# Kernel tuning notes

Measured on AMD Instinct MI355X. Metric: run time of the kernel, lower is better.

The kernel has to match this reference:

```python
import jax, jax.numpy as jnp
import numpy as np

D_MODEL = 1024
N_HEADS = 16
DEPTH = D_MODEL // N_HEADS  # 64
BATCH, SEQ = 4, 2048


def setup_inputs() -> dict:
    key = jax.random.key(0)
    ks = jax.random.split(key, 8)
    x = jax.random.normal(ks[0], (BATCH, SEQ, D_MODEL), dtype=jnp.float32)
    # Per-head Dense(depth) weights stacked over heads: [H, d_model, depth]
    s = 1.0 / np.sqrt(D_MODEL)
    Wq = jax.random.normal(ks[1], (N_HEADS, D_MODEL, DEPTH), dtype=jnp.float32) * s
    Wk = jax.random.normal(ks[2], (N_HEADS, D_MODEL, DEPTH), dtype=jnp.float32) * s
    Wv = jax.random.normal(ks[3], (N_HEADS, D_MODEL, DEPTH), dtype=jnp.float32) * s
    bq = jnp.zeros((N_HEADS, DEPTH), dtype=jnp.float32)
    bk = jnp.zeros((N_HEADS, DEPTH), dtype=jnp.float32)
    bv = jnp.zeros((N_HEADS, DEPTH), dtype=jnp.float32)
    Wo = jax.random.normal(ks[4], (D_MODEL, D_MODEL), dtype=jnp.float32) * s
    bo = jnp.zeros((D_MODEL,), dtype=jnp.float32)
    return {"x": x, "Wq": Wq, "bq": bq, "Wk": Wk, "bk": bk,
            "Wv": Wv, "bv": bv, "Wo": Wo, "bo": bo}


def reference(x, Wq, bq, Wk, bk, Wv, bv, Wo, bo):
    # Per-head projections, batched over heads: [b, h, s, depth]
    q = jnp.einsum('bsd,hde->bhse', x, Wq) + bq[None, :, None, :]
    k = jnp.einsum('bsd,hde->bhse', x, Wk) + bk[None, :, None, :]
    v = jnp.einsum('bsd,hde->bhse', x, Wv) + bv[None, :, None, :]
    scale = 1.0 / jnp.sqrt(jnp.float32(DEPTH))
    scores = jnp.einsum('bhqe,bhke->bhqk', q, k) * scale  # [b, h, s, s]
    attn = jax.nn.softmax(scores, axis=-1)
    z = jnp.einsum('bhqk,bhke->bhqe', attn, v)  # [b, h, s, depth]
    # Concat heads along last axis (head-major order matches tf.concat of per-head outputs)
    multi_head = z.transpose(0, 2, 1, 3).reshape(BATCH, SEQ, D_MODEL)
    return multi_head @ Wo + bo
```

## Files before the change

kernel.cpp:

```cpp
#include <hip/hip_runtime.h>

typedef unsigned short u16;
typedef __bf16 bf16x8 __attribute__((ext_vector_type(8)));
typedef float f32x4 __attribute__((ext_vector_type(4)));
typedef float f32x16 __attribute__((ext_vector_type(16)));
typedef unsigned int u32x4 __attribute__((ext_vector_type(4)));
typedef unsigned int u32x2 __attribute__((ext_vector_type(2)));

__device__ __forceinline__ u16 f2b(float f) {
  union { float f; unsigned u; } v; v.f = f;
  return (u16)((v.u + 0x7fffu + ((v.u >> 16) & 1u)) >> 16);
}

__device__ __forceinline__ unsigned pkbf(float a, float b) {
#if __has_builtin(__builtin_amdgcn_cvt_pk_bf16_f32)
  typedef __bf16 bf16x2v __attribute__((ext_vector_type(2)));
  bf16x2v r = __builtin_amdgcn_cvt_pk_bf16_f32(a, b);
  return __builtin_bit_cast(unsigned, r);
#else
  unsigned ua = __builtin_bit_cast(unsigned, a) + 0x8000u;
  unsigned ub = __builtin_bit_cast(unsigned, b) + 0x8000u;
  return __builtin_amdgcn_perm(ub, ua, 0x07060302u);
#endif
}

__device__ __forceinline__ float fexp2(float x) {
#if __has_builtin(__builtin_amdgcn_exp2f)
  return __builtin_amdgcn_exp2f(x);
#else
  return exp2f(x);
#endif
}

__device__ __forceinline__ bf16x8 ldfrag(const u16* p) {
  u32x4 r = *(const u32x4*)p;
  return __builtin_bit_cast(bf16x8, r);
}

__device__ __forceinline__ void plswap(unsigned& dst, unsigned& src) {
  asm("v_permlane32_swap_b32 %0, %1" : "+v"(dst), "+v"(src));
}

__device__ __forceinline__ float sum16(const f32x16& v) {
  float a = (v[0] + v[1]) + (v[2] + v[3]);
  float b = (v[4] + v[5]) + (v[6] + v[7]);
  float c = (v[8] + v[9]) + (v[10] + v[11]);
  float d = (v[12] + v[13]) + (v[14] + v[15]);
  return (a + b) + (c + d);
}

__device__ __forceinline__ void build_frags(const f32x16& sc, bf16x8& fLo, bf16x8& fHi) {
  unsigned a0 = pkbf(sc[0], sc[1]);
  unsigned a1 = pkbf(sc[2], sc[3]);
  unsigned b0 = pkbf(sc[4], sc[5]);
  unsigned b1 = pkbf(sc[6], sc[7]);
  plswap(a0, b0);
  plswap(a1, b1);
  u32x4 f; f[0] = a0; f[1] = a1; f[2] = b0; f[3] = b1;
  fLo = __builtin_bit_cast(bf16x8, f);
  unsigned c0 = pkbf(sc[8], sc[9]);
  unsigned c1 = pkbf(sc[10], sc[11]);
  unsigned d0 = pkbf(sc[12], sc[13]);
  unsigned d1 = pkbf(sc[14], sc[15]);
  plswap(c0, d0);
  plswap(c1, d1);
  u32x4 g; g[0] = c0; g[1] = c1; g[2] = d0; g[3] = d1;
  fHi = __builtin_bit_cast(bf16x8, g);
}

#define GLOAD_LDS16(gp, lp)                                                        \
  __builtin_amdgcn_global_load_lds((const __attribute__((address_space(1))) void*)(gp), \
                                   (__attribute__((address_space(3))) void*)(lp), 16, 0, 0)

#define MFMA32(a, b, c) __builtin_amdgcn_mfma_f32_32x32x16_bf16((a), (b), (c), 0, 0, 0)

#define QSC 0.18033688011f


__global__ __launch_bounds__(256) void k_pack(const float* __restrict__ x,
                                              const float* __restrict__ Wq,
                                              const float* __restrict__ Wk,
                                              const float* __restrict__ Wv,
                                              const float* __restrict__ Wo,
                                              u16* __restrict__ xb,
                                              u16* __restrict__ wqkv,
                                              u16* __restrict__ wo_t) {
  const int bid = blockIdx.x, tid = threadIdx.x;
  if (bid < 4096) {
    int i = (bid * 256 + tid) * 8;
    float4 v0 = *(const float4*)(x + i);
    float4 v1 = *(const float4*)(x + i + 4);
    u32x4 o;
    o[0] = pkbf(v0.x, v0.y);
    o[1] = pkbf(v0.z, v0.w);
    o[2] = pkbf(v1.x, v1.y);
    o[3] = pkbf(v1.z, v1.w);
    *(u32x4*)(xb + i) = o;
    return;
  }
  __shared__ u16 tile[64][65];
  if (bid < 4864) {
    int b2 = bid - 4096;
    int p = b2 >> 8, rem = b2 & 255, h = rem >> 4, dt = rem & 15;
    const float* W = (p == 0) ? Wq : (p == 1) ? Wk : Wv;
    for (int i = tid; i < 4096; i += 256) {
      int d = i >> 6, e = i & 63;
      tile[e][d] = f2b(W[h * 65536 + (dt * 64 + d) * 64 + e]);
    }
    __syncthreads();
    for (int i = tid; i < 4096; i += 256) {
      int e = i >> 6, d = i & 63;
      wqkv[(size_t)(p * 1024 + h * 64 + e) * 1024 + dt * 64 + d] = tile[e][d];
    }
  } else {
    int b2 = bid - 4864;
    int kt = b2 >> 4, nt = b2 & 15;
    for (int i = tid; i < 4096; i += 256) {
      int dk = i >> 6, de = i & 63;
      tile[de][dk] = f2b(Wo[(size_t)(kt * 64 + dk) * 1024 + nt * 64 + de]);
    }
    __syncthreads();
    for (int i = tid; i < 4096; i += 256) {
      int de = i >> 6, dk = i & 63;
      wo_t[(size_t)(nt * 64 + de) * 1024 + kt * 64 + dk] = tile[de][dk];
    }
  }
}


template <bool SWAP>
__device__ __forceinline__ void gemm_core32(const u16* __restrict__ A, const u16* __restrict__ Bt,
                                            int row0, int col0, u16* As, u16* Bs, f32x16 acc[2][2]) {
  const int tid = threadIdx.x, w = tid >> 6, lane = tid & 63;
  const int l31 = lane & 31, hi = lane >> 5;
  const int wm = (w >> 1) * 64, wn = (w & 1) * 64;
  for (int k0 = 0; k0 < 1024; k0 += 32) {
#pragma unroll
    for (int i = 0; i < 2; i++) {
      int bse = (w * 2 + i) * 512;
      int flat = bse + lane * 8;
      int r = flat >> 5, c = flat & 31;
      GLOAD_LDS16(A + (size_t)(row0 + r) * 1024 + k0 + c, As + bse);
      GLOAD_LDS16(Bt + (size_t)(col0 + r) * 1024 + k0 + c, Bs + bse);
    }
    __syncthreads();
    bf16x8 af[2][2], bfr[2][2];
#pragma unroll
    for (int t = 0; t < 2; t++)
#pragma unroll
      for (int s = 0; s < 2; s++) {
        af[t][s] = ldfrag(As + (wm + t * 32 + l31) * 32 + s * 16 + hi * 8);
        bfr[t][s] = ldfrag(Bs + (wn + t * 32 + l31) * 32 + s * 16 + hi * 8);
      }
#pragma unroll
    for (int mt = 0; mt < 2; mt++)
#pragma unroll
      for (int nt = 0; nt < 2; nt++)
#pragma unroll
        for (int s = 0; s < 2; s++)
          acc[mt][nt] = SWAP ? MFMA32(bfr[nt][s], af[mt][s], acc[mt][nt])
                             : MFMA32(af[mt][s], bfr[nt][s], acc[mt][nt]);
    __syncthreads();
  }
}


__global__ __launch_bounds__(256) void k_gemm_qkv(const u16* __restrict__ xb, const u16* __restrict__ wt,
                                                  const float* __restrict__ bq, const float* __restrict__ bk,
                                                  const float* __restrict__ bv,
                                                  u16* __restrict__ qo, u16* __restrict__ ko,
                                                  u16* __restrict__ vto) {
  __shared__ u16 As[4096], Bs[4096];
  f32x16 acc[2][2];
#pragma unroll
  for (int a = 0; a < 2; a++)
#pragma unroll
    for (int b = 0; b < 2; b++)
#pragma unroll
      for (int r = 0; r < 16; r++) acc[a][b][r] = 0.f;

  const int row0 = blockIdx.x * 128, col0 = blockIdx.y * 128;
  const int p = blockIdx.y >> 3;
  const int colr = (blockIdx.y & 7) * 128;
  const int tid = threadIdx.x, w = tid >> 6, lane = tid & 63;
  const int l31 = lane & 31, hi = lane >> 5;
  const int wm = (w >> 1) * 64, wn = (w & 1) * 64;

  if (p == 2) {
    gemm_core32<true>(xb, wt, row0, col0, As, Bs, acc);
#pragma unroll
    for (int mt = 0; mt < 2; mt++) {
      int rb = row0 + wm + mt * 32;
      int b_ = rb >> 11;
      int s_ = (rb & 2047) + l31;
#pragma unroll
      for (int nt = 0; nt < 2; nt++) {
        int ebase = colr + wn + nt * 32;
#pragma unroll
        for (int g = 0; g < 4; g++) {
          float4 bvv = *(const float4*)(bv + ebase + g * 8 + hi * 4);
#pragma unroll
          for (int j = 0; j < 4; j++) {
            int rem = ebase + g * 8 + hi * 4 + j;
            int h = rem >> 6, e = rem & 63;
            float val = acc[mt][nt][g * 4 + j] + (&bvv.x)[j];
            vto[(((size_t)(b_ * 16 + h)) * 64 + e) * 2048 + s_] = f2b(val);
          }
        }
      }
    }
  } else {
    gemm_core32<false>(xb, wt, row0, col0, As, Bs, acc);
    u16* dst = (p == 0) ? qo : ko;
    const float* bias = (p == 0) ? bq : bk;
    const float qsc = (p == 0) ? QSC : 1.0f;
#pragma unroll
    for (int nt = 0; nt < 2; nt++) {
      int rem = colr + wn + nt * 32 + l31;
      int h = rem >> 6, e = rem & 63;
      float bval = bias[rem];
#pragma unroll
      for (int mt = 0; mt < 2; mt++) {
        int rb = row0 + wm + mt * 32;
        int b_ = rb >> 11, sb = rb & 2047;
        size_t obase = ((size_t)(b_ * 16 + h) * 2048) * 64 + e;
#pragma unroll
        for (int reg = 0; reg < 16; reg++) {
          int s_ = sb + (reg & 3) + 8 * (reg >> 2) + 4 * hi;
          float val = (acc[mt][nt][reg] + bval) * qsc;
          dst[obase + (size_t)s_ * 64] = f2b(val);
        }
      }
    }
  }
}


__global__ __launch_bounds__(256) void k_gemm_out(const u16* __restrict__ zb, const u16* __restrict__ wt,
                                                  const float* __restrict__ bo, float* __restrict__ out) {
  __shared__ u16 As[4096], Bs[4096];
  f32x16 acc[2][2];
#pragma unroll
  for (int a = 0; a < 2; a++)
#pragma unroll
    for (int b = 0; b < 2; b++)
#pragma unroll
      for (int r = 0; r < 16; r++) acc[a][b][r] = 0.f;

  const int row0 = blockIdx.x * 128, col0 = blockIdx.y * 128;
  gemm_core32<false>(zb, wt, row0, col0, As, Bs, acc);

  const int tid = threadIdx.x, w = tid >> 6, lane = tid & 63;
  const int l31 = lane & 31, hi = lane >> 5;
  const int wm = (w >> 1) * 64, wn = (w & 1) * 64;
#pragma unroll
  for (int nt = 0; nt < 2; nt++) {
    int c = col0 + wn + nt * 32 + l31;
    float bval = bo[c];
#pragma unroll
    for (int mt = 0; mt < 2; mt++) {
      int rb = row0 + wm + mt * 32;
#pragma unroll
      for (int reg = 0; reg < 16; reg++) {
        int r = rb + (reg & 3) + 8 * (reg >> 2) + 4 * hi;
        out[(size_t)r * 1024 + c] = acc[mt][nt][reg] + bval;
      }
    }
  }
}


__global__ __launch_bounds__(256, 2) void k_attn(const u16* __restrict__ q, const u16* __restrict__ k,
                                                 const u16* __restrict__ vt, u16* __restrict__ z) {
  __shared__ u16 Ks[2][64 * 72], Vs[2][64 * 72];
  const int tid = threadIdx.x, w = tid >> 6, lane = tid & 63;
  const int l31 = lane & 31, hi = lane >> 5;
  const int bh = blockIdx.y, s0 = blockIdx.x * 256;
  const size_t base = (size_t)bh * 2048 * 64;
  const int qrow0 = s0 + w * 64;

  bf16x8 qf[2][4];
#pragma unroll
  for (int u = 0; u < 2; u++) {
    const u16* qp = q + base + (size_t)(qrow0 + u * 32 + l31) * 64 + hi * 8;
#pragma unroll
    for (int ks = 0; ks < 4; ks++) qf[u][ks] = ldfrag(qp + ks * 16);
  }

  f32x16 accT[2][2];
  float ls[2] = {0.f, 0.f};
#pragma unroll
  for (int u = 0; u < 2; u++)
#pragma unroll
    for (int r = 0; r < 16; r++) { accT[u][0][r] = 0.f; accT[u][1][r] = 0.f; }

  const int srow = tid >> 3;
  const int scol = (tid & 7) * 8;
  const u16* kg = k + base;
  const u16* vg = vt + base;

  u32x4 kr0 = *(const u32x4*)(kg + (size_t)srow * 64 + scol);
  u32x4 kr1 = *(const u32x4*)(kg + (size_t)(srow + 32) * 64 + scol);
  u32x4 vr0 = *(const u32x4*)(vg + (size_t)srow * 2048 + scol);
  u32x4 vr1 = *(const u32x4*)(vg + (size_t)(srow + 32) * 2048 + scol);
  *(u32x4*)&Ks[0][srow * 72 + scol] = kr0;
  *(u32x4*)&Ks[0][(srow + 32) * 72 + scol] = kr1;
  *(u32x4*)&Vs[0][srow * 72 + scol] = vr0;
  *(u32x4*)&Vs[0][(srow + 32) * 72 + scol] = vr1;
  kr0 = *(const u32x4*)(kg + (size_t)(64 + srow) * 64 + scol);
  kr1 = *(const u32x4*)(kg + (size_t)(64 + srow + 32) * 64 + scol);
  vr0 = *(const u32x4*)(vg + (size_t)srow * 2048 + 64 + scol);
  vr1 = *(const u32x4*)(vg + (size_t)(srow + 32) * 2048 + 64 + scol);
  __syncthreads();

  for (int kc = 0; kc < 2048; kc += 64) {
    const int buf = (kc >> 6) & 1;
    const u16* Kb = &Ks[buf][0];
    const u16* Vb = &Vs[buf][0];

    bf16x8 pf[2][4];
#pragma unroll
    for (int t = 0; t < 2; t++) {
      f32x16 scA, scB;
#pragma unroll
      for (int r = 0; r < 16; r++) { scA[r] = 0.f; scB[r] = 0.f; }
      __builtin_amdgcn_s_setprio(1);
#pragma unroll
      for (int ks = 0; ks < 4; ks++) {
        bf16x8 kf = ldfrag(Kb + (t * 32 + l31) * 72 + ks * 16 + hi * 8);
        scA = MFMA32(kf, qf[0][ks], scA);
        scB = MFMA32(kf, qf[1][ks], scB);
      }
      __builtin_amdgcn_s_setprio(0);
#pragma unroll
      for (int r = 0; r < 16; r++) scA[r] = fexp2(scA[r]);
#pragma unroll
      for (int r = 0; r < 16; r++) scB[r] = fexp2(scB[r]);
      ls[0] += sum16(scA);
      ls[1] += sum16(scB);
      build_frags(scA, pf[0][2 * t], pf[0][2 * t + 1]);
      build_frags(scB, pf[1][2 * t], pf[1][2 * t + 1]);
    }

    if (kc + 64 < 2048) {
      *(u32x4*)&Ks[buf ^ 1][srow * 72 + scol] = kr0;
      *(u32x4*)&Ks[buf ^ 1][(srow + 32) * 72 + scol] = kr1;
      *(u32x4*)&Vs[buf ^ 1][srow * 72 + scol] = vr0;
      *(u32x4*)&Vs[buf ^ 1][(srow + 32) * 72 + scol] = vr1;
      if (kc + 128 < 2048) {
        int kn = kc + 128;
        kr0 = *(const u32x4*)(kg + (size_t)(kn + srow) * 64 + scol);
        kr1 = *(const u32x4*)(kg + (size_t)(kn + srow + 32) * 64 + scol);
        vr0 = *(const u32x4*)(vg + (size_t)srow * 2048 + kn + scol);
        vr1 = *(const u32x4*)(vg + (size_t)(srow + 32) * 2048 + kn + scol);
      }
    }

    __builtin_amdgcn_s_setprio(1);
#pragma unroll
    for (int ks = 0; ks < 4; ks++) {
      bf16x8 vf0 = ldfrag(Vb + (0 * 32 + l31) * 72 + ks * 16 + hi * 8);
      bf16x8 vf1 = ldfrag(Vb + (1 * 32 + l31) * 72 + ks * 16 + hi * 8);
      accT[0][0] = MFMA32(vf0, pf[0][ks], accT[0][0]);
      accT[0][1] = MFMA32(vf1, pf[0][ks], accT[0][1]);
      accT[1][0] = MFMA32(vf0, pf[1][ks], accT[1][0]);
      accT[1][1] = MFMA32(vf1, pf[1][ks], accT[1][1]);
    }
    __builtin_amdgcn_s_setprio(0);
    __syncthreads();
  }

  const int b_ = bh >> 4, h = bh & 15;
#pragma unroll
  for (int u = 0; u < 2; u++) {
    float l = ls[u];
    l += __shfl_xor(l, 32);
    float inv = 1.f / l;
    int qrow = qrow0 + u * 32 + l31;
    u16* zr = z + ((size_t)(b_ * 2048 + qrow)) * 1024 + h * 64;
#pragma unroll
    for (int et = 0; et < 2; et++)
#pragma unroll
      for (int rr = 0; rr < 16; rr += 2) {
        unsigned pkd = pkbf(accT[u][et][rr] * inv, accT[u][et][rr + 1] * inv);
        int e = et * 32 + (rr & 3) + 8 * (rr >> 2) + 4 * hi;
        *(unsigned*)&zr[e] = pkd;
      }
  }
}


extern "C" void kernel_launch(void* const* d_in, const int* in_sizes, int n_in,
                              void* d_out, int out_size, void* d_ws, size_t ws_size,
                              hipStream_t stream) {
  (void)in_sizes; (void)n_in; (void)out_size;
  const float* x  = (const float*)d_in[0];
  const float* Wq = (const float*)d_in[1];
  const float* bq = (const float*)d_in[2];
  const float* Wk = (const float*)d_in[3];
  const float* bk = (const float*)d_in[4];
  const float* Wv = (const float*)d_in[5];
  const float* bv = (const float*)d_in[6];
  const float* Wo = (const float*)d_in[7];
  const float* bo = (const float*)d_in[8];
  float* out = (float*)d_out;
  char* ws = (char*)d_ws;
  if (ws_size < 92274688u) return;

  u16* xb   = (u16*)(ws + 0);
  u16* wqkv = (u16*)(ws + 16777216);
  u16* wo_t = (u16*)(ws + 23068672);
  u16* qb   = (u16*)(ws + 25165824);
  u16* kb   = (u16*)(ws + 41943040);
  u16* vtb  = (u16*)(ws + 58720256);
  u16* zb   = (u16*)(ws + 75497472);

  k_pack<<<5120, 256, 0, stream>>>(x, Wq, Wk, Wv, Wo, xb, wqkv, wo_t);
  k_gemm_qkv<<<dim3(64, 24), 256, 0, stream>>>(xb, wqkv, bq, bk, bv, qb, kb, vtb);
  k_attn<<<dim3(8, 64), 256, 0, stream>>>(qb, kb, vtb, zb);
  k_gemm_out<<<dim3(64, 8), 256, 0, stream>>>(zb, wo_t, bo, out);
}
```

Baseline: 290.3 us.

## Double-buffer GEMM LDS tiles with XOR swizzle and MFMA priority

The shared GEMM core used by the QKV projection and output projection now double-buffers its LDS tiles. It prefetches the next k-slice with direct global-to-LDS loads while MFMAs run on the current one, which drops one barrier per iteration. The LDS layout gets an XOR swizzle on 16-byte chunks to cut bank conflicts in fragment reads, and s_setprio raises wave priority around the MFMA block. LDS use per block doubles, which may lower occupancy. Correctness relies on the swizzle offsets matching between the global-to-LDS writes and the fragment reads.

```diff
diff --git a/kernel.cpp b/kernel.cpp
--- a/kernel.cpp
+++ b/kernel.cpp
@@ -134,24 +134,58 @@
   const int tid = threadIdx.x, w = tid >> 6, lane = tid & 63;
   const int l31 = lane & 31, hi = lane >> 5;
   const int wm = (w >> 1) * 64, wn = (w & 1) * 64;
+
+  int r_[2], c_[2];
+#pragma unroll
+  for (int i = 0; i < 2; i++) {
+    int X = (w * 2 + i) * 1024 + lane * 16;
+    int e = (X ^ (((X >> 7) & 7) << 4)) >> 1;
+    r_[i] = e >> 5;
+    c_[i] = e & 31;
+  }
+  int oa[2][2], ob[2][2];
+#pragma unroll
+  for (int t = 0; t < 2; t++)
+#pragma unroll
+    for (int s = 0; s < 2; s++) {
+      int Pa = (wm + t * 32 + l31) * 64 + s * 32 + hi * 16;
+      int Pb = (wn + t * 32 + l31) * 64 + s * 32 + hi * 16;
+      oa[t][s] = (Pa ^ (((Pa >> 7) & 7) << 4)) >> 1;
+      ob[t][s] = (Pb ^ (((Pb >> 7) & 7) << 4)) >> 1;
+    }
+
+  const u16* Ag = A + (size_t)row0 * 1024;
+  const u16* Bg = Bt + (size_t)col0 * 1024;
+
+#pragma unroll
+  for (int i = 0; i < 2; i++) {
+    GLOAD_LDS16(Ag + (size_t)r_[i] * 1024 + c_[i], As + (w * 2 + i) * 512);
+    GLOAD_LDS16(Bg + (size_t)r_[i] * 1024 + c_[i], Bs + (w * 2 + i) * 512);
+  }
+  __syncthreads();
+
+  int cur = 0;
   for (int k0 = 0; k0 < 1024; k0 += 32) {
-#pragma unroll
-    for (int i = 0; i < 2; i++) {
-      int bse = (w * 2 + i) * 512;
-      int flat = bse + lane * 8;
-      int r = flat >> 5, c = flat & 31;
-      GLOAD_LDS16(A + (size_t)(row0 + r) * 1024 + k0 + c, As + bse);
-      GLOAD_LDS16(Bt + (size_t)(col0 + r) * 1024 + k0 + c, Bs + bse);
-    }
-    __syncthreads();
+    if (k0 + 32 < 1024) {
+      u16* Ad = As + (cur ^ 1) * 4096 + (w * 2) * 512;
+      u16* Bd = Bs + (cur ^ 1) * 4096 + (w * 2) * 512;
+#pragma unroll
+      for (int i = 0; i < 2; i++) {
+        GLOAD_LDS16(Ag + (size_t)r_[i] * 1024 + k0 + 32 + c_[i], Ad + i * 512);
+        GLOAD_LDS16(Bg + (size_t)r_[i] * 1024 + k0 + 32 + c_[i], Bd + i * 512);
+      }
+    }
+    const u16* Ab = As + cur * 4096;
+    const u16* Bb = Bs + cur * 4096;
     bf16x8 af[2][2], bfr[2][2];
 #pragma unroll
     for (int t = 0; t < 2; t++)
 #pragma unroll
       for (int s = 0; s < 2; s++) {
-        af[t][s] = ldfrag(As + (wm + t * 32 + l31) * 32 + s * 16 + hi * 8);
-        bfr[t][s] = ldfrag(Bs + (wn + t * 32 + l31) * 32 + s * 16 + hi * 8);
-      }
+        af[t][s] = ldfrag(Ab + oa[t][s]);
+        bfr[t][s] = ldfrag(Bb + ob[t][s]);
+      }
+    __builtin_amdgcn_s_setprio(1);
 #pragma unroll
     for (int mt = 0; mt < 2; mt++)
 #pragma unroll
@@ -160,7 +194,9 @@
         for (int s = 0; s < 2; s++)
           acc[mt][nt] = SWAP ? MFMA32(bfr[nt][s], af[mt][s], acc[mt][nt])
                              : MFMA32(af[mt][s], bfr[nt][s], acc[mt][nt]);
+    __builtin_amdgcn_s_setprio(0);
     __syncthreads();
+    cur ^= 1;
   }
 }
 
@@ -170,7 +206,7 @@
                                                   const float* __restrict__ bv,
                                                   u16* __restrict__ qo, u16* __restrict__ ko,
                                                   u16* __restrict__ vto) {
-  __shared__ u16 As[4096], Bs[4096];
+  __shared__ u16 As[8192], Bs[8192];
   f32x16 acc[2][2];
 #pragma unroll
   for (int a = 0; a < 2; a++)
@@ -238,7 +274,7 @@
 
 __global__ __launch_bounds__(256) void k_gemm_out(const u16* __restrict__ zb, const u16* __restrict__ wt,
                                                   const float* __restrict__ bo, float* __restrict__ out) {
-  __shared__ u16 As[4096], Bs[4096];
+  __shared__ u16 As[8192], Bs[8192];
   f32x16 acc[2][2];
 #pragma unroll
   for (int a = 0; a < 2; a++)
```

New measurement: 285.1 us. Within noise of the previous version (-1.8%).

## Pipeline GEMM K-loop with 4-stage swizzled LDS buffers and reorder attention grid

Applied to the files above, without the earlier changes.

Replaces the synchronous GEMM core, which did load, sync, compute, sync on each step, with a four-buffer LDS ring. Loads run two steps ahead, and waits use vmcnt counts plus a single barrier per iteration. The LDS layout gets an XOR swizzle to cut bank conflicts on fragment reads, and MFMA sections are wrapped in setprio. The attention grid is also transposed so consecutive blocks cover different heads instead of different query tiles of the same head. This raises LDS use to 64KB per GEMM block, which may lower occupancy.

```diff
diff --git a/kernel.cpp b/kernel.cpp
--- a/kernel.cpp
+++ b/kernel.cpp
@@ -128,40 +128,83 @@
 }
 
 
+#define PIPE_WAIT(n)                                      \
+  asm volatile("s_waitcnt vmcnt(" #n ")" ::: "memory");   \
+  __builtin_amdgcn_s_barrier();                           \
+  __builtin_amdgcn_sched_barrier(0);
+
 template <bool SWAP>
-__device__ __forceinline__ void gemm_core32(const u16* __restrict__ A, const u16* __restrict__ Bt,
-                                            int row0, int col0, u16* As, u16* Bs, f32x16 acc[2][2]) {
+__device__ __forceinline__ void gemm_core32q(const u16* __restrict__ A, const u16* __restrict__ Bt,
+                                             int row0, int col0, u16* As, u16* Bs, f32x16 acc[2][2]) {
   const int tid = threadIdx.x, w = tid >> 6, lane = tid & 63;
   const int l31 = lane & 31, hi = lane >> 5;
   const int wm = (w >> 1) * 64, wn = (w & 1) * 64;
-  for (int k0 = 0; k0 < 1024; k0 += 32) {
-#pragma unroll
-    for (int i = 0; i < 2; i++) {
-      int bse = (w * 2 + i) * 512;
-      int flat = bse + lane * 8;
-      int r = flat >> 5, c = flat & 31;
-      GLOAD_LDS16(A + (size_t)(row0 + r) * 1024 + k0 + c, As + bse);
-      GLOAD_LDS16(Bt + (size_t)(col0 + r) * 1024 + k0 + c, Bs + bse);
-    }
-    __syncthreads();
-    bf16x8 af[2][2], bfr[2][2];
-#pragma unroll
-    for (int t = 0; t < 2; t++)
-#pragma unroll
-      for (int s = 0; s < 2; s++) {
-        af[t][s] = ldfrag(As + (wm + t * 32 + l31) * 32 + s * 16 + hi * 8);
-        bfr[t][s] = ldfrag(Bs + (wn + t * 32 + l31) * 32 + s * 16 + hi * 8);
-      }
-#pragma unroll
-    for (int mt = 0; mt < 2; mt++)
-#pragma unroll
-      for (int nt = 0; nt < 2; nt++)
-#pragma unroll
-        for (int s = 0; s < 2; s++)
-          acc[mt][nt] = SWAP ? MFMA32(bfr[nt][s], af[mt][s], acc[mt][nt])
-                             : MFMA32(af[mt][s], bfr[nt][s], acc[mt][nt]);
-    __syncthreads();
-  }
+
+  int r_[2], c_[2];
+#pragma unroll
+  for (int i = 0; i < 2; i++) {
+    int X = (w * 2 + i) * 1024 + lane * 16;
+    int e = (X ^ (((X >> 7) & 7) << 4)) >> 1;
+    r_[i] = e >> 5;
+    c_[i] = e & 31;
+  }
+  int oa[2][2], ob[2][2];
+#pragma unroll
+  for (int t = 0; t < 2; t++)
+#pragma unroll
+    for (int s = 0; s < 2; s++) {
+      int Pa = (wm + t * 32 + l31) * 64 + s * 32 + hi * 16;
+      int Pb = (wn + t * 32 + l31) * 64 + s * 32 + hi * 16;
+      oa[t][s] = (Pa ^ (((Pa >> 7) & 7) << 4)) >> 1;
+      ob[t][s] = (Pb ^ (((Pb >> 7) & 7) << 4)) >> 1;
+    }
+
+  const u16* Ag = A + (size_t)row0 * 1024;
+  const u16* Bg = Bt + (size_t)col0 * 1024;
+
+#define PIPE_ISSUE(k2)                                                              \
+  {                                                                                 \
+    u16* Ad = As + ((k2) & 3) * 4096 + (w * 2) * 512;                               \
+    u16* Bd = Bs + ((k2) & 3) * 4096 + (w * 2) * 512;                               \
+    _Pragma("unroll") for (int i = 0; i < 2; i++) {                                 \
+      GLOAD_LDS16(Ag + (size_t)r_[i] * 1024 + (k2) * 32 + c_[i], Ad + i * 512);     \
+      GLOAD_LDS16(Bg + (size_t)r_[i] * 1024 + (k2) * 32 + c_[i], Bd + i * 512);     \
+    }                                                                               \
+  }
+
+#define PIPE_COMPUTE(it)                                                            \
+  {                                                                                 \
+    const u16* Ab = As + ((it) & 3) * 4096;                                         \
+    const u16* Bb = Bs + ((it) & 3) * 4096;                                         \
+    bf16x8 af[2][2], bfr[2][2];                                                     \
+    _Pragma("unroll") for (int t = 0; t < 2; t++)                                   \
+      _Pragma("unroll") for (int s = 0; s < 2; s++) {                               \
+        af[t][s] = ldfrag(Ab + oa[t][s]);                                           \
+        bfr[t][s] = ldfrag(Bb + ob[t][s]);                                          \
+      }                                                                             \
+    __builtin_amdgcn_s_setprio(1);                                                  \
+    _Pragma("unroll") for (int mt = 0; mt < 2; mt++)                                \
+      _Pragma("unroll") for (int nt = 0; nt < 2; nt++)                              \
+        _Pragma("unroll") for (int s = 0; s < 2; s++)                               \
+          acc[mt][nt] = SWAP ? MFMA32(bfr[nt][s], af[mt][s], acc[mt][nt])           \
+                             : MFMA32(af[mt][s], bfr[nt][s], acc[mt][nt]);          \
+    __builtin_amdgcn_s_setprio(0);                                                  \
+  }
+
+  PIPE_ISSUE(0);
+  PIPE_ISSUE(1);
+  for (int it = 0; it < 30; ++it) {
+    PIPE_ISSUE(it + 2);
+    PIPE_WAIT(8)
+    PIPE_COMPUTE(it);
+  }
+  PIPE_WAIT(4)
+  PIPE_COMPUTE(30);
+  PIPE_WAIT(0)
+  PIPE_COMPUTE(31);
+
+#undef PIPE_ISSUE
+#undef PIPE_COMPUTE
 }
 
 
@@ -170,7 +213,7 @@
                                                   const float* __restrict__ bv,
                                                   u16* __restrict__ qo, u16* __restrict__ ko,
                                                   u16* __restrict__ vto) {
-  __shared__ u16 As[4096], Bs[4096];
+  __shared__ u16 As[16384], Bs[16384];
   f32x16 acc[2][2];
 #pragma unroll
   for (int a = 0; a < 2; a++)
@@ -187,7 +230,7 @@
   const int wm = (w >> 1) * 64, wn = (w & 1) * 64;
 
   if (p == 2) {
-    gemm_core32<true>(xb, wt, row0, col0, As, Bs, acc);
+    gemm_core32q<true>(xb, wt, row0, col0, As, Bs, acc);
 #pragma unroll
     for (int mt = 0; mt < 2; mt++) {
       int rb = row0 + wm + mt * 32;
@@ -210,7 +253,7 @@
       }
     }
   } else {
-    gemm_core32<false>(xb, wt, row0, col0, As, Bs, acc);
+    gemm_core32q<false>(xb, wt, row0, col0, As, Bs, acc);
     u16* dst = (p == 0) ? qo : ko;
     const float* bias = (p == 0) ? bq : bk;
     const float qsc = (p == 0) ? QSC : 1.0f;
@@ -238,7 +281,7 @@
 
 __global__ __launch_bounds__(256) void k_gemm_out(const u16* __restrict__ zb, const u16* __restrict__ wt,
                                                   const float* __restrict__ bo, float* __restrict__ out) {
-  __shared__ u16 As[4096], Bs[4096];
+  __shared__ u16 As[16384], Bs[16384];
   f32x16 acc[2][2];
 #pragma unroll
   for (int a = 0; a < 2; a++)
@@ -248,7 +291,7 @@
       for (int r = 0; r < 16; r++) acc[a][b][r] = 0.f;
 
   const int row0 = blockIdx.x * 128, col0 = blockIdx.y * 128;
-  gemm_core32<false>(zb, wt, row0, col0, As, Bs, acc);
+  gemm_core32q<false>(zb, wt, row0, col0, As, Bs, acc);
 
   const int tid = threadIdx.x, w = tid >> 6, lane = tid & 63;
   const int l31 = lane & 31, hi = lane >> 5;
@@ -275,7 +318,7 @@
   __shared__ u16 Ks[2][64 * 72], Vs[2][64 * 72];
   const int tid = threadIdx.x, w = tid >> 6, lane = tid & 63;
   const int l31 = lane & 31, hi = lane >> 5;
-  const int bh = blockIdx.y, s0 = blockIdx.x * 256;
+  const int bh = blockIdx.x, s0 = blockIdx.y * 256;
   const size_t base = (size_t)bh * 2048 * 64;
   const int qrow0 = s0 + w * 64;
 
@@ -417,6 +460,6 @@
 
   k_pack<<<5120, 256, 0, stream>>>(x, Wq, Wk, Wv, Wo, xb, wqkv, wo_t);
   k_gemm_qkv<<<dim3(64, 24), 256, 0, stream>>>(xb, wqkv, bq, bk, bv, qb, kb, vtb);
-  k_attn<<<dim3(8, 64), 256, 0, stream>>>(qb, kb, vtb, zb);
+  k_attn<<<dim3(64, 8), 256, 0, stream>>>(qb, kb, vtb, zb);
   k_gemm_out<<<dim3(64, 8), 256, 0, stream>>>(zb, wo_t, bo, out);
 }
```

Measured after the change: 287.0 us. Within noise of the previous version (-1.1%).
